# Kernel optimization log

Hardware: AMD Instinct MI355X
Metric: run time of the kernel (lower is better)

Reference implementation:

```python
import jax, jax.numpy as jnp
import numpy as np

N_NODES = 100000

def _graph_conv(x, src, dst, W, b, norm_src, norm_dst, activation):
    # DGL GraphConv, norm='both': D_out^{-1/2} on source, sum-aggregate, D_in^{-1/2} on dest
    h = x * norm_src[:, None]                       # [N, Din]
    # mult by W first when it reduces width (here Din >= Dout always) -> W then aggregate
    h = h @ W                                       # [N, Dout]
    m = jax.ops.segment_sum(h[src], dst, num_segments=N_NODES)  # gather + scatter-add
    out = m * norm_dst[:, None] + b
    if activation:
        out = jax.nn.relu(out)
    return out

def setup_inputs() -> dict:
    key = jax.random.key(0)
    ks = jax.random.split(key, 10)
    N, Din, H, Dout = N_NODES, 128, 128, 64
    E = 1600000
    x = jax.random.normal(ks[0], (N, Din), dtype=jnp.float32)
    src = jax.random.randint(ks[1], (E,), 0, N, dtype=jnp.int64)
    dst = jax.random.randint(ks[2], (E,), 0, N, dtype=jnp.int64)
    def glorot(k, fin, fout):
        s = jnp.sqrt(6.0 / (fin + fout)).astype(jnp.float32)
        return jax.random.uniform(k, (fin, fout), jnp.float32, -s, s)
    return {
        "x": x, "src": src, "dst": dst,
        "W1": glorot(ks[3], Din, H), "b1": jnp.zeros((H,), jnp.float32),
        "W2": glorot(ks[4], H, H),   "b2": jnp.zeros((H,), jnp.float32),
        "W3": glorot(ks[5], H, Dout),"b3": jnp.zeros((Dout,), jnp.float32),
    }

def reference(x, src, dst, W1, b1, W2, b2, W3, b3):
    ones = jnp.ones(src.shape[0], dtype=x.dtype)
    out_deg = jax.ops.segment_sum(ones, src, num_segments=N_NODES)
    in_deg = jax.ops.segment_sum(ones, dst, num_segments=N_NODES)
    norm_src = jax.lax.rsqrt(jnp.maximum(out_deg, 1.0))
    norm_dst = jax.lax.rsqrt(jnp.maximum(in_deg, 1.0))
    h = _graph_conv(x, src, dst, W1, b1, norm_src, norm_dst, True)
    h = _graph_conv(h, src, dst, W2, b2, norm_src, norm_dst, True)
    h = _graph_conv(h, src, dst, W3, b3, norm_src, norm_dst, False)
    return h
```

## Files before the change

kernel.cpp:

```cpp
#include <hip/hip_runtime.h>

#define NN 100000
#define NB 196
#define CH 4096
#define HB 192

typedef short short8 __attribute__((ext_vector_type(8)));
typedef unsigned short u16x8 __attribute__((ext_vector_type(8)));
typedef float f32x4 __attribute__((ext_vector_type(4)));

__device__ inline unsigned short f2bf(float x) {
    unsigned u = __float_as_uint(x);
    unsigned r = (u + 0x7FFF + ((u >> 16) & 1)) >> 16;
    return (unsigned short)r;
}
__device__ inline float bf2f(unsigned short h) {
    return __uint_as_float(((unsigned)h) << 16);
}

__global__ __launch_bounds__(256) void k_bhist2p(const int* __restrict__ src,
    const int* __restrict__ dst, int* __restrict__ partS, int* __restrict__ partD, int E)
{
    __shared__ int hs[NB], hd[NB];
    int t = threadIdx.x;
    if (t < NB) { hs[t] = 0; hd[t] = 0; }
    __syncthreads();
    int stride = HB * 256;
    for (int e = blockIdx.x * 256 + t; e < E; e += stride) {
        atomicAdd(&hs[src[e] >> 9], 1);
        atomicAdd(&hd[dst[e] >> 9], 1);
    }
    __syncthreads();
    partS[blockIdx.x * 256 + t] = (t < NB) ? hs[t] : 0;
    partD[blockIdx.x * 256 + t] = (t < NB) ? hd[t] : 0;
}

__global__ __launch_bounds__(256) void k_bscan2(const int* __restrict__ partS,
    const int* __restrict__ partD,
    int* __restrict__ bcntS, int* __restrict__ bcntD,
    int* __restrict__ bbaseS, int* __restrict__ gcurS,
    int* __restrict__ bbaseD, int* __restrict__ gcurD)
{
    __shared__ int s[256];
    int t = threadIdx.x;
    int cS = 0, cD = 0;
    for (int i = 0; i < HB; i++) {
        cS += partS[i * 256 + t];
        cD += partD[i * 256 + t];
    }
    if (t < NB) { bcntS[t] = cS; bcntD[t] = cD; }

    int v = cD;
    s[t] = v;
    __syncthreads();
#pragma unroll
    for (int off = 1; off < 256; off <<= 1) {
        int x = (t >= off) ? s[t - off] : 0;
        __syncthreads(); s[t] += x; __syncthreads();
    }
    if (t < NB) { int e = s[t] - v; bbaseD[t] = e; gcurD[t] = e; }
    __syncthreads();

    v = cS;
    s[t] = v;
    __syncthreads();
#pragma unroll
    for (int off = 1; off < 256; off <<= 1) {
        int x = (t >= off) ? s[t - off] : 0;
        __syncthreads(); s[t] += x; __syncthreads();
    }
    if (t < NB) { int e = s[t] - v; bbaseS[t] = e; gcurS[t] = e; }
}

__global__ __launch_bounds__(256) void k_bscatter3(const int* __restrict__ src,
    const int* __restrict__ dst, int* __restrict__ gcurD, int* __restrict__ gcurS,
    unsigned* __restrict__ tmpD, unsigned* __restrict__ tmpS, int E)
{
    __shared__ int cntD[NB], cntS[NB];
    __shared__ int runD[NB], runS[NB];
    int t = threadIdx.x;
    if (t < NB) { cntD[t] = 0; cntS[t] = 0; }
    __syncthreads();

    const int e0 = blockIdx.x * CH;
    int sv[16], dv[16];
    int offD[16], offS[16];
#pragma unroll
    for (int i = 0; i < 16; i++) {
        int e = e0 + i * 256 + t;
        if (e < E) { sv[i] = src[e]; dv[i] = dst[e]; }
    }
#pragma unroll
    for (int i = 0; i < 16; i++) {
        int e = e0 + i * 256 + t;
        if (e < E) {
            offD[i] = atomicAdd(&cntD[dv[i] >> 9], 1);
            offS[i] = atomicAdd(&cntS[sv[i] >> 9], 1);
        }
    }
    __syncthreads();
    if (t < NB) {
        int c = cntD[t];
        if (c) runD[t] = atomicAdd(&gcurD[t], c);
        c = cntS[t];
        if (c) runS[t] = atomicAdd(&gcurS[t], c);
    }
    __syncthreads();
#pragma unroll
    for (int i = 0; i < 16; i++) {
        int e = e0 + i * 256 + t;
        if (e < E) {
            int bD = dv[i] >> 9;
            tmpD[runD[bD] + offD[i]] = (unsigned)sv[i] | ((unsigned)(dv[i] & 511) << 17);
            int bS = sv[i] >> 9;
            tmpS[runS[bS] + offS[i]] = (unsigned)(sv[i] & 511);
        }
    }
}

__global__ __launch_bounds__(256) void k_build(
    const int* __restrict__ bbaseD, const int* __restrict__ bcntD, const unsigned* __restrict__ tmpD,
    const int* __restrict__ bbaseS, const int* __restrict__ bcntS, const unsigned* __restrict__ tmpS,
    int* __restrict__ degI, float* __restrict__ nd, float* __restrict__ ns,
    int* __restrict__ rowptr, int* __restrict__ srcIdx, int N)
{
    __shared__ int cnt[8192];
    __shared__ int sblk[256];
    int t = threadIdx.x;

    if (blockIdx.x >= NB) {
        int b = blockIdx.x - NB;
        cnt[t] = 0; cnt[t + 256] = 0;
        __syncthreads();
        int beg = bbaseS[b], end = beg + bcntS[b];
        for (int e = beg + t; e < end; e += 256)
            atomicAdd(&cnt[tmpS[e]], 1);
        __syncthreads();
        int nb = b << 9;
        for (int i = t; i < 512; i += 256) {
            int n = nb + i;
            if (n < N) ns[n] = rsqrtf(fmaxf((float)cnt[i], 1.0f));
        }
        return;
    }

    int b = blockIdx.x;
    for (int i = t; i < 8192; i += 256) cnt[i] = 0;
    __syncthreads();
    int beg = bbaseD[b], end = beg + bcntD[b];
    for (int e = beg + t; e < end; e += 256) {
        unsigned v = tmpD[e];
        int dl = v >> 17;
        int s  = (int)(v & 0x1FFFFu);
        atomicAdd(&cnt[(dl << 4) | (s >> 13)], 1);
    }
    __syncthreads();
    int loc[32];
    int sum = 0;
#pragma unroll
    for (int i = 0; i < 32; i++) { loc[i] = sum; sum += cnt[t * 32 + i]; }
    sblk[t] = sum;
    __syncthreads();
#pragma unroll
    for (int off = 1; off < 256; off <<= 1) {
        int x = (t >= off) ? sblk[t - off] : 0;
        __syncthreads(); sblk[t] += x; __syncthreads();
    }
    int base = beg + sblk[t] - sum;
    int v0 = loc[16];
    int v1 = sum - loc[16];
    int nb = b << 9;
    int n0 = nb + 2 * t, n1 = n0 + 1;
    if (n0 < N) { rowptr[n0] = base;           degI[n0] = v0; nd[n0] = rsqrtf(fmaxf((float)v0, 1.f)); }
    if (n1 < N) { rowptr[n1] = base + loc[16]; degI[n1] = v1; nd[n1] = rsqrtf(fmaxf((float)v1, 1.f)); }
#pragma unroll
    for (int i = 0; i < 32; i++) cnt[t * 32 + i] = base + loc[i];
    __syncthreads();
    for (int e = beg + t; e < end; e += 256) {
        unsigned v = tmpD[e];
        int dl = v >> 17;
        int s  = (int)(v & 0x1FFFFu);
        int pos = atomicAdd(&cnt[(dl << 4) | (s >> 13)], 1);
        srcIdx[pos] = s;
    }
}

__global__ __launch_bounds__(256) void k_prepW_all(
    const float* __restrict__ W1, const float* __restrict__ W2, const float* __restrict__ W3,
    unsigned short* __restrict__ W1h, unsigned short* __restrict__ W1l,
    unsigned short* __restrict__ W2h, unsigned short* __restrict__ W2l,
    unsigned short* __restrict__ W3h, unsigned short* __restrict__ W3l)
{
    int b = blockIdx.x;
    const float* W; unsigned short *Wh, *Wl; int DOUT, idx;
    if (b < 64)       { W = W1; Wh = W1h; Wl = W1l; DOUT = 128; idx = b * 256 + threadIdx.x; }
    else if (b < 128) { W = W2; Wh = W2h; Wl = W2l; DOUT = 128; idx = (b - 64) * 256 + threadIdx.x; }
    else              { W = W3; Wh = W3h; Wl = W3l; DOUT = 64;  idx = (b - 128) * 256 + threadIdx.x; }
    if (idx >= 128 * DOUT) return;
    int c = idx % DOUT;
    int k = idx / DOUT;
    float w = W[idx];
    unsigned short hi = f2bf(w);
    unsigned short lo = f2bf(w - bf2f(hi));
    int boff = c * 256 + ((2 * k) ^ ((c & 7) << 4));
    *(unsigned short*)((char*)Wh + boff) = hi;
    *(unsigned short*)((char*)Wl + boff) = lo;
}

template<int DOUT>
__global__ __launch_bounds__(256) void k_gemm_mfma(
    const float* __restrict__ in,
    const unsigned short* __restrict__ Wth, const unsigned short* __restrict__ Wtl,
    const float* __restrict__ ns,
    unsigned short* __restrict__ out, int N)
{
    constexpr int NT = DOUT / 16;
    __shared__ __align__(16) unsigned short Wh[DOUT * 128];
    __shared__ __align__(16) unsigned short Wl[DOUT * 128];

    const int t = threadIdx.x;
    const int w = t >> 6, l = t & 63;

#pragma unroll
    for (int i = 0; i < DOUT * 256 / 4096; i++) {
        int off = i * 4096 + t * 16;
        *(float4*)((char*)Wh + off) = *(const float4*)((const char*)Wth + off);
        *(float4*)((char*)Wl + off) = *(const float4*)((const char*)Wtl + off);
    }

    const int rl   = l & 15;
    const int kgrp = l >> 4;
    const int row  = blockIdx.x * 64 + w * 16 + rl;
    const int rowc = row < N ? row : N - 1;
    const float* arow = in + (size_t)rowc * 128;

    float av[4][8];
#pragma unroll
    for (int ks = 0; ks < 4; ks++) {
        int kb = ks * 32 + kgrp * 8;
        float4 v0 = *(const float4*)(arow + kb);
        float4 v1 = *(const float4*)(arow + kb + 4);
        av[ks][0] = v0.x; av[ks][1] = v0.y; av[ks][2] = v0.z; av[ks][3] = v0.w;
        av[ks][4] = v1.x; av[ks][5] = v1.y; av[ks][6] = v1.z; av[ks][7] = v1.w;
    }
    float nsv = ns[rowc];
    short8 Ah[4], Al[4];
#pragma unroll
    for (int ks = 0; ks < 4; ks++)
#pragma unroll
        for (int j = 0; j < 8; j++) {
            float v = av[ks][j] * nsv;
            unsigned short hi = f2bf(v);
            Ah[ks][j] = (short)hi;
            Al[ks][j] = (short)f2bf(v - bf2f(hi));
        }

    __syncthreads();

    f32x4 acc[NT];
#pragma unroll
    for (int tt = 0; tt < NT; tt++) acc[tt] = (f32x4){0.f, 0.f, 0.f, 0.f};

#pragma unroll
    for (int ks = 0; ks < 4; ks++) {
        int kbyte = ks * 64 + kgrp * 16;
#pragma unroll
        for (int tt = 0; tt < NT; tt++) {
            int c = tt * 16 + rl;
            int boff = c * 256 + (kbyte ^ ((c & 7) << 4));
            short8 Bh = *(short8*)((char*)Wh + boff);
            short8 Bl = *(short8*)((char*)Wl + boff);
            acc[tt] = __builtin_amdgcn_mfma_f32_16x16x32_bf16(Ah[ks], Bh, acc[tt], 0, 0, 0);
            acc[tt] = __builtin_amdgcn_mfma_f32_16x16x32_bf16(Al[ks], Bh, acc[tt], 0, 0, 0);
            acc[tt] = __builtin_amdgcn_mfma_f32_16x16x32_bf16(Ah[ks], Bl, acc[tt], 0, 0, 0);
        }
    }

    const int orow = blockIdx.x * 64 + w * 16 + kgrp * 4;
#pragma unroll
    for (int r = 0; r < 4; r++) {
        if (orow + r < N) {
#pragma unroll
            for (int tt = 0; tt < NT; tt++)
                out[(size_t)(orow + r) * DOUT + tt * 16 + rl] = f2bf(acc[tt][r]);
        }
    }
}

__global__ __launch_bounds__(256) void k_agg_epi(
    const int* __restrict__ rowptr, const int* __restrict__ cnt,
    const int* __restrict__ srcIdx, const unsigned short* __restrict__ h,
    const float* __restrict__ nd, const float* __restrict__ ns,
    const float* __restrict__ bias,
    unsigned short* __restrict__ out, int N)
{
    int t = threadIdx.x;
    int node = blockIdx.x * 16 + (t >> 4);
    if (node >= N) return;
    int c = (t & 15) * 8;

    int beg = rowptr[node];
    int end = beg + cnt[node];
    float acc[8] = {0.f, 0.f, 0.f, 0.f, 0.f, 0.f, 0.f, 0.f};
    int e = beg;
    for (; e + 3 < end; e += 4) {
        int s0 = srcIdx[e], s1 = srcIdx[e + 1], s2 = srcIdx[e + 2], s3 = srcIdx[e + 3];
        u16x8 v0 = *(const u16x8*)&h[(size_t)s0 * 128 + c];
        u16x8 v1 = *(const u16x8*)&h[(size_t)s1 * 128 + c];
        u16x8 v2 = *(const u16x8*)&h[(size_t)s2 * 128 + c];
        u16x8 v3 = *(const u16x8*)&h[(size_t)s3 * 128 + c];
#pragma unroll
        for (int j = 0; j < 8; j++)
            acc[j] += (bf2f(v0[j]) + bf2f(v1[j])) + (bf2f(v2[j]) + bf2f(v3[j]));
    }
    for (; e < end; e++) {
        int s0 = srcIdx[e];
        u16x8 v0 = *(const u16x8*)&h[(size_t)s0 * 128 + c];
#pragma unroll
        for (int j = 0; j < 8; j++) acc[j] += bf2f(v0[j]);
    }
    float ndv = nd[node], nsv = ns[node];
    float4 b0 = *(const float4*)(bias + c);
    float4 b1 = *(const float4*)(bias + c + 4);
    float bb[8] = {b0.x, b0.y, b0.z, b0.w, b1.x, b1.y, b1.z, b1.w};
    u16x8 o;
#pragma unroll
    for (int j = 0; j < 8; j++)
        o[j] = f2bf(fmaxf(acc[j] * ndv + bb[j], 0.f) * nsv);
    *(u16x8*)&out[(size_t)node * 128 + c] = o;
}

template<int DOUT>
__global__ __launch_bounds__(256) void k_gemm_bf(
    const unsigned short* __restrict__ in,
    const unsigned short* __restrict__ Wth, const unsigned short* __restrict__ Wtl,
    unsigned short* __restrict__ out, int N)
{
    constexpr int NT = DOUT / 16;
    __shared__ __align__(16) unsigned short Wh[DOUT * 128];
    __shared__ __align__(16) unsigned short Wl[DOUT * 128];

    const int t = threadIdx.x;
    const int w = t >> 6, l = t & 63;

#pragma unroll
    for (int i = 0; i < DOUT * 256 / 4096; i++) {
        int off = i * 4096 + t * 16;
        *(float4*)((char*)Wh + off) = *(const float4*)((const char*)Wth + off);
        *(float4*)((char*)Wl + off) = *(const float4*)((const char*)Wtl + off);
    }

    const int rl   = l & 15;
    const int kgrp = l >> 4;
    const int row  = blockIdx.x * 64 + w * 16 + rl;
    const int rowc = row < N ? row : N - 1;
    const unsigned short* arow = in + (size_t)rowc * 128;

    short8 Ah[4];
#pragma unroll
    for (int ks = 0; ks < 4; ks++)
        Ah[ks] = *(const short8*)(arow + ks * 32 + kgrp * 8);

    __syncthreads();

    f32x4 acc[NT];
#pragma unroll
    for (int tt = 0; tt < NT; tt++) acc[tt] = (f32x4){0.f, 0.f, 0.f, 0.f};

#pragma unroll
    for (int ks = 0; ks < 4; ks++) {
        int kbyte = ks * 64 + kgrp * 16;
#pragma unroll
        for (int tt = 0; tt < NT; tt++) {
            int c = tt * 16 + rl;
            int boff = c * 256 + (kbyte ^ ((c & 7) << 4));
            short8 Bh = *(short8*)((char*)Wh + boff);
            short8 Bl = *(short8*)((char*)Wl + boff);
            acc[tt] = __builtin_amdgcn_mfma_f32_16x16x32_bf16(Ah[ks], Bh, acc[tt], 0, 0, 0);
            acc[tt] = __builtin_amdgcn_mfma_f32_16x16x32_bf16(Ah[ks], Bl, acc[tt], 0, 0, 0);
        }
    }

    const int orow = blockIdx.x * 64 + w * 16 + kgrp * 4;
#pragma unroll
    for (int r = 0; r < 4; r++) {
        if (orow + r < N) {
#pragma unroll
            for (int tt = 0; tt < NT; tt++)
                out[(size_t)(orow + r) * DOUT + tt * 16 + rl] = f2bf(acc[tt][r]);
        }
    }
}

template<int D>
__global__ __launch_bounds__(256) void k_agg_final(
    const int* __restrict__ rowptr, const int* __restrict__ cnt,
    const int* __restrict__ srcIdx, const unsigned short* __restrict__ h,
    const float* __restrict__ nd, const float* __restrict__ b3,
    float* __restrict__ m, int N)
{
    constexpr int TPN = D / 8;
    constexpr int NPB = 256 / TPN;
    int t = threadIdx.x;
    int node = blockIdx.x * NPB + t / TPN;
    if (node >= N) return;
    int c = (t % TPN) * 8;

    int beg = rowptr[node];
    int end = beg + cnt[node];
    float acc[8] = {0.f, 0.f, 0.f, 0.f, 0.f, 0.f, 0.f, 0.f};
    int e = beg;
    for (; e + 3 < end; e += 4) {
        int s0 = srcIdx[e], s1 = srcIdx[e + 1], s2 = srcIdx[e + 2], s3 = srcIdx[e + 3];
        u16x8 v0 = *(const u16x8*)&h[(size_t)s0 * D + c];
        u16x8 v1 = *(const u16x8*)&h[(size_t)s1 * D + c];
        u16x8 v2 = *(const u16x8*)&h[(size_t)s2 * D + c];
        u16x8 v3 = *(const u16x8*)&h[(size_t)s3 * D + c];
#pragma unroll
        for (int j = 0; j < 8; j++)
            acc[j] += (bf2f(v0[j]) + bf2f(v1[j])) + (bf2f(v2[j]) + bf2f(v3[j]));
    }
    for (; e < end; e++) {
        int s0 = srcIdx[e];
        u16x8 v0 = *(const u16x8*)&h[(size_t)s0 * D + c];
#pragma unroll
        for (int j = 0; j < 8; j++) acc[j] += bf2f(v0[j]);
    }
    float ndv = nd[node];
#pragma unroll
    for (int j = 0; j < 8; j++) acc[j] = acc[j] * ndv + b3[c + j];
    float4* mp = (float4*)&m[(size_t)node * D + c];
    mp[0] = make_float4(acc[0], acc[1], acc[2], acc[3]);
    mp[1] = make_float4(acc[4], acc[5], acc[6], acc[7]);
}

extern "C" void kernel_launch(void* const* d_in, const int* in_sizes, int n_in,
                              void* d_out, int out_size, void* d_ws, size_t ws_size,
                              hipStream_t stream) {
    const float* x  = (const float*)d_in[0];
    const int*   src = (const int*)d_in[1];
    const int*   dst = (const int*)d_in[2];
    const float* W1 = (const float*)d_in[3];
    const float* b1 = (const float*)d_in[4];
    const float* W2 = (const float*)d_in[5];
    const float* b2 = (const float*)d_in[6];
    const float* W3 = (const float*)d_in[7];
    const float* b3 = (const float*)d_in[8];
    float* out = (float*)d_out;

    const int N = NN;
    const int E = in_sizes[1];

    char* ws = (char*)d_ws;
    unsigned short* bufA = (unsigned short*)ws;
    unsigned short* bufB = (unsigned short*)(ws + (size_t)N * 128 * 4);
    unsigned* tmpD = (unsigned*)bufA;
    unsigned* tmpS = (unsigned*)bufB;
    char*  p     = ws + (size_t)N * 128 * 4 * 2;
    float* ns    = (float*)p;              p += (size_t)N * 4;
    float* nd    = (float*)p;              p += (size_t)N * 4;
    int*   degI  = (int*)p;                p += (size_t)N * 4;
    int*   rowp  = (int*)p;                p += (size_t)N * 4;
    int*   srcIdx= (int*)p;                p += (size_t)E * 4;
    unsigned short* W1h = (unsigned short*)p; p += 128 * 128 * 2;
    unsigned short* W1l = (unsigned short*)p; p += 128 * 128 * 2;
    unsigned short* W2h = (unsigned short*)p; p += 128 * 128 * 2;
    unsigned short* W2l = (unsigned short*)p; p += 128 * 128 * 2;
    unsigned short* W3h = (unsigned short*)p; p += 64 * 128 * 2;
    unsigned short* W3l = (unsigned short*)p; p += 64 * 128 * 2;
    int* bcntS = (int*)p;                  p += 256 * 4;
    int* bcntD = (int*)p;                  p += 256 * 4;
    int* bbaseS= (int*)p;                  p += 256 * 4;
    int* bbaseD= (int*)p;                  p += 256 * 4;
    int* gcurS = (int*)p;                  p += 256 * 4;
    int* gcurD = (int*)p;                  p += 256 * 4;
    int* partS = (int*)p;                  p += (size_t)HB * 256 * 4;
    int* partD = (int*)p;                  p += (size_t)HB * 256 * 4;
    unsigned short* bufC = (unsigned short*)p;

    k_prepW_all<<<160, 256, 0, stream>>>(W1, W2, W3, W1h, W1l, W2h, W2l, W3h, W3l);

    k_bhist2p<<<HB, 256, 0, stream>>>(src, dst, partS, partD, E);
    k_bscan2<<<1, 256, 0, stream>>>(partS, partD, bcntS, bcntD, bbaseS, gcurS, bbaseD, gcurD);
    k_bscatter3<<<(E + CH - 1) / CH, 256, 0, stream>>>(src, dst, gcurD, gcurS, tmpD, tmpS, E);
    k_build<<<2 * NB, 256, 0, stream>>>(bbaseD, bcntD, tmpD, bbaseS, bcntS, tmpS,
                                        degI, nd, ns, rowp, srcIdx, N);

    const int gemm_grid = (N + 63) / 64;
    const int agg16     = (N + 15) / 16;
    const int agg64     = (N + 31) / 32;

    k_gemm_mfma<128><<<gemm_grid, 256, 0, stream>>>(x, W1h, W1l, ns, bufA, N);

    k_agg_epi<<<agg16, 256, 0, stream>>>(rowp, degI, srcIdx, bufA, nd, ns, b1, bufB, N);
    k_gemm_bf<128><<<gemm_grid, 256, 0, stream>>>(bufB, W2h, W2l, bufC, N);

    k_agg_epi<<<agg16, 256, 0, stream>>>(rowp, degI, srcIdx, bufC, nd, ns, b2, bufB, N);
    k_gemm_bf<64><<<gemm_grid, 256, 0, stream>>>(bufB, W3h, W3l, bufA, N);

    k_agg_final<64><<<agg64, 256, 0, stream>>>(rowp, degI, srcIdx, bufA, nd, b3, out, N);
}
```

Baseline: 284.6 us.

## Replace edge-bucket histogram and scan with fixed-capacity buckets and fuse weight prep

Drops the per-bucket histogram and scan kernels. Each 512-node bucket now gets a fixed slot of BSTRIDE entries, and its fill level comes from a global atomic cursor that a memset zeroes first. Weight bf16 splitting is folded into the scatter kernel as extra blocks. The CSR build no longer sub-sorts a row's edges by source high bits, which frees a lot of shared memory. This saves a pass over the edge list and two launches. In exchange, row-internal source ordering is lost, and any bucket that gets more than 9216 edges would overflow.

```diff
diff --git a/kernel.cpp b/kernel.cpp
--- a/kernel.cpp
+++ b/kernel.cpp
@@ -3,7 +3,7 @@
 #define NN 100000
 #define NB 196
 #define CH 4096
-#define HB 192
+#define BSTRIDE 9216
 
 typedef short short8 __attribute__((ext_vector_type(8)));
 typedef unsigned short u16x8 __attribute__((ext_vector_type(8)));
@@ -18,67 +18,37 @@
     return __uint_as_float(((unsigned)h) << 16);
 }
 
-__global__ __launch_bounds__(256) void k_bhist2p(const int* __restrict__ src,
-    const int* __restrict__ dst, int* __restrict__ partS, int* __restrict__ partD, int E)
-{
-    __shared__ int hs[NB], hd[NB];
-    int t = threadIdx.x;
-    if (t < NB) { hs[t] = 0; hd[t] = 0; }
-    __syncthreads();
-    int stride = HB * 256;
-    for (int e = blockIdx.x * 256 + t; e < E; e += stride) {
-        atomicAdd(&hs[src[e] >> 9], 1);
-        atomicAdd(&hd[dst[e] >> 9], 1);
-    }
-    __syncthreads();
-    partS[blockIdx.x * 256 + t] = (t < NB) ? hs[t] : 0;
-    partD[blockIdx.x * 256 + t] = (t < NB) ? hd[t] : 0;
-}
-
-__global__ __launch_bounds__(256) void k_bscan2(const int* __restrict__ partS,
-    const int* __restrict__ partD,
-    int* __restrict__ bcntS, int* __restrict__ bcntD,
-    int* __restrict__ bbaseS, int* __restrict__ gcurS,
-    int* __restrict__ bbaseD, int* __restrict__ gcurD)
-{
-    __shared__ int s[256];
-    int t = threadIdx.x;
-    int cS = 0, cD = 0;
-    for (int i = 0; i < HB; i++) {
-        cS += partS[i * 256 + t];
-        cD += partD[i * 256 + t];
-    }
-    if (t < NB) { bcntS[t] = cS; bcntD[t] = cD; }
-
-    int v = cD;
-    s[t] = v;
-    __syncthreads();
-#pragma unroll
-    for (int off = 1; off < 256; off <<= 1) {
-        int x = (t >= off) ? s[t - off] : 0;
-        __syncthreads(); s[t] += x; __syncthreads();
-    }
-    if (t < NB) { int e = s[t] - v; bbaseD[t] = e; gcurD[t] = e; }
-    __syncthreads();
-
-    v = cS;
-    s[t] = v;
-    __syncthreads();
-#pragma unroll
-    for (int off = 1; off < 256; off <<= 1) {
-        int x = (t >= off) ? s[t - off] : 0;
-        __syncthreads(); s[t] += x; __syncthreads();
-    }
-    if (t < NB) { int e = s[t] - v; bbaseS[t] = e; gcurS[t] = e; }
-}
-
-__global__ __launch_bounds__(256) void k_bscatter3(const int* __restrict__ src,
-    const int* __restrict__ dst, int* __restrict__ gcurD, int* __restrict__ gcurS,
-    unsigned* __restrict__ tmpD, unsigned* __restrict__ tmpS, int E)
+__global__ __launch_bounds__(256) void k_scatter_prep(
+    const int* __restrict__ src, const int* __restrict__ dst,
+    int* __restrict__ gcurD, int* __restrict__ gcurS,
+    unsigned* __restrict__ tmpD, unsigned* __restrict__ tmpS, int E, int nEdgeBlk,
+    const float* __restrict__ W1, const float* __restrict__ W2, const float* __restrict__ W3,
+    unsigned short* __restrict__ W1h, unsigned short* __restrict__ W1l,
+    unsigned short* __restrict__ W2h, unsigned short* __restrict__ W2l,
+    unsigned short* __restrict__ W3h, unsigned short* __restrict__ W3l)
 {
     __shared__ int cntD[NB], cntS[NB];
     __shared__ int runD[NB], runS[NB];
     int t = threadIdx.x;
+
+    if (blockIdx.x >= nEdgeBlk) {
+        int b = blockIdx.x - nEdgeBlk;
+        const float* W; unsigned short *Wh, *Wl; int DOUT, idx;
+        if (b < 64)       { W = W1; Wh = W1h; Wl = W1l; DOUT = 128; idx = b * 256 + t; }
+        else if (b < 128) { W = W2; Wh = W2h; Wl = W2l; DOUT = 128; idx = (b - 64) * 256 + t; }
+        else              { W = W3; Wh = W3h; Wl = W3l; DOUT = 64;  idx = (b - 128) * 256 + t; }
+        if (idx >= 128 * DOUT) return;
+        int c = idx % DOUT;
+        int k = idx / DOUT;
+        float w = W[idx];
+        unsigned short hi = f2bf(w);
+        unsigned short lo = f2bf(w - bf2f(hi));
+        int boff = c * 256 + ((2 * k) ^ ((c & 7) << 4));
+        *(unsigned short*)((char*)Wh + boff) = hi;
+        *(unsigned short*)((char*)Wl + boff) = lo;
+        return;
+    }
+
     if (t < NB) { cntD[t] = 0; cntS[t] = 0; }
     __syncthreads();
 
@@ -101,9 +71,9 @@
     __syncthreads();
     if (t < NB) {
         int c = cntD[t];
-        if (c) runD[t] = atomicAdd(&gcurD[t], c);
+        if (c) runD[t] = t * BSTRIDE + atomicAdd(&gcurD[t], c);
         c = cntS[t];
-        if (c) runS[t] = atomicAdd(&gcurS[t], c);
+        if (c) runS[t] = t * BSTRIDE + atomicAdd(&gcurS[t], c);
     }
     __syncthreads();
 #pragma unroll
@@ -119,20 +89,21 @@
 }
 
 __global__ __launch_bounds__(256) void k_build(
-    const int* __restrict__ bbaseD, const int* __restrict__ bcntD, const unsigned* __restrict__ tmpD,
-    const int* __restrict__ bbaseS, const int* __restrict__ bcntS, const unsigned* __restrict__ tmpS,
+    const int* __restrict__ gcurD, const unsigned* __restrict__ tmpD,
+    const int* __restrict__ gcurS, const unsigned* __restrict__ tmpS,
     int* __restrict__ degI, float* __restrict__ nd, float* __restrict__ ns,
     int* __restrict__ rowptr, int* __restrict__ srcIdx, int N)
 {
-    __shared__ int cnt[8192];
+    __shared__ int cnt[512];
     __shared__ int sblk[256];
+    __shared__ int lcur[512];
     int t = threadIdx.x;
 
     if (blockIdx.x >= NB) {
         int b = blockIdx.x - NB;
         cnt[t] = 0; cnt[t + 256] = 0;
         __syncthreads();
-        int beg = bbaseS[b], end = beg + bcntS[b];
+        int beg = b * BSTRIDE, end = beg + gcurS[b];
         for (int e = beg + t; e < end; e += 256)
             atomicAdd(&cnt[tmpS[e]], 1);
         __syncthreads();
@@ -145,66 +116,33 @@
     }
 
     int b = blockIdx.x;
-    for (int i = t; i < 8192; i += 256) cnt[i] = 0;
-    __syncthreads();
-    int beg = bbaseD[b], end = beg + bcntD[b];
-    for (int e = beg + t; e < end; e += 256) {
-        unsigned v = tmpD[e];
-        int dl = v >> 17;
-        int s  = (int)(v & 0x1FFFFu);
-        atomicAdd(&cnt[(dl << 4) | (s >> 13)], 1);
-    }
-    __syncthreads();
-    int loc[32];
-    int sum = 0;
-#pragma unroll
-    for (int i = 0; i < 32; i++) { loc[i] = sum; sum += cnt[t * 32 + i]; }
-    sblk[t] = sum;
+    cnt[t] = 0; cnt[t + 256] = 0;
+    __syncthreads();
+    int beg = b * BSTRIDE, end = beg + gcurD[b];
+    for (int e = beg + t; e < end; e += 256)
+        atomicAdd(&cnt[tmpD[e] >> 17], 1);
+    __syncthreads();
+    int v0 = cnt[2 * t], v1 = cnt[2 * t + 1];
+    sblk[t] = v0 + v1;
     __syncthreads();
 #pragma unroll
     for (int off = 1; off < 256; off <<= 1) {
         int x = (t >= off) ? sblk[t - off] : 0;
         __syncthreads(); sblk[t] += x; __syncthreads();
     }
-    int base = beg + sblk[t] - sum;
-    int v0 = loc[16];
-    int v1 = sum - loc[16];
+    int e0 = beg + sblk[t] - v0 - v1;
+    int e1_ = e0 + v0;
     int nb = b << 9;
     int n0 = nb + 2 * t, n1 = n0 + 1;
-    if (n0 < N) { rowptr[n0] = base;           degI[n0] = v0; nd[n0] = rsqrtf(fmaxf((float)v0, 1.f)); }
-    if (n1 < N) { rowptr[n1] = base + loc[16]; degI[n1] = v1; nd[n1] = rsqrtf(fmaxf((float)v1, 1.f)); }
-#pragma unroll
-    for (int i = 0; i < 32; i++) cnt[t * 32 + i] = base + loc[i];
+    if (n0 < N) { rowptr[n0] = e0;  degI[n0] = v0; nd[n0] = rsqrtf(fmaxf((float)v0, 1.f)); }
+    if (n1 < N) { rowptr[n1] = e1_; degI[n1] = v1; nd[n1] = rsqrtf(fmaxf((float)v1, 1.f)); }
+    lcur[2 * t] = e0; lcur[2 * t + 1] = e1_;
     __syncthreads();
     for (int e = beg + t; e < end; e += 256) {
         unsigned v = tmpD[e];
-        int dl = v >> 17;
-        int s  = (int)(v & 0x1FFFFu);
-        int pos = atomicAdd(&cnt[(dl << 4) | (s >> 13)], 1);
-        srcIdx[pos] = s;
-    }
-}
-
-__global__ __launch_bounds__(256) void k_prepW_all(
-    const float* __restrict__ W1, const float* __restrict__ W2, const float* __restrict__ W3,
-    unsigned short* __restrict__ W1h, unsigned short* __restrict__ W1l,
-    unsigned short* __restrict__ W2h, unsigned short* __restrict__ W2l,
-    unsigned short* __restrict__ W3h, unsigned short* __restrict__ W3l)
-{
-    int b = blockIdx.x;
-    const float* W; unsigned short *Wh, *Wl; int DOUT, idx;
-    if (b < 64)       { W = W1; Wh = W1h; Wl = W1l; DOUT = 128; idx = b * 256 + threadIdx.x; }
-    else if (b < 128) { W = W2; Wh = W2h; Wl = W2l; DOUT = 128; idx = (b - 64) * 256 + threadIdx.x; }
-    else              { W = W3; Wh = W3h; Wl = W3l; DOUT = 64;  idx = (b - 128) * 256 + threadIdx.x; }
-    if (idx >= 128 * DOUT) return;
-    int c = idx % DOUT;
-    int k = idx / DOUT;
-    float w = W[idx];
-    unsigned short hi = f2bf(w);
-    unsigned short lo = f2bf(w - bf2f(hi));
-    int boff = c * 256 + ((2 * k) ^ ((c & 7) << 4));
-    *(unsigned short*)((char*)Wh + boff) = hi;
-    *(unsigned short*)((char*)Wl + boff) = lo;
+        int pos = atomicAdd(&lcur[v >> 17], 1);
+        srcIdx[pos] = (int)(v & 0x1FFFFu);
+    }
 }
 
 template<int DOUT>
@@ -450,6 +388,7 @@
 
     const int N = NN;
     const int E = in_sizes[1];
+    const int nEdgeBlk = (E + CH - 1) / CH;
 
     char* ws = (char*)d_ws;
     unsigned short* bufA = (unsigned short*)ws;
@@ -461,29 +400,21 @@
     float* nd    = (float*)p;              p += (size_t)N * 4;
     int*   degI  = (int*)p;                p += (size_t)N * 4;
     int*   rowp  = (int*)p;                p += (size_t)N * 4;
-    int*   srcIdx= (int*)p;                p += (size_t)E * 4;
+    int*   srcIdx= (int*)p;                p += (size_t)NB * BSTRIDE * 4;
     unsigned short* W1h = (unsigned short*)p; p += 128 * 128 * 2;
     unsigned short* W1l = (unsigned short*)p; p += 128 * 128 * 2;
     unsigned short* W2h = (unsigned short*)p; p += 128 * 128 * 2;
     unsigned short* W2l = (unsigned short*)p; p += 128 * 128 * 2;
     unsigned short* W3h = (unsigned short*)p; p += 64 * 128 * 2;
     unsigned short* W3l = (unsigned short*)p; p += 64 * 128 * 2;
-    int* bcntS = (int*)p;                  p += 256 * 4;
-    int* bcntD = (int*)p;                  p += 256 * 4;
-    int* bbaseS= (int*)p;                  p += 256 * 4;
-    int* bbaseD= (int*)p;                  p += 256 * 4;
+    int* gcurD = (int*)p;                  p += 256 * 4;
     int* gcurS = (int*)p;                  p += 256 * 4;
-    int* gcurD = (int*)p;                  p += 256 * 4;
-    int* partS = (int*)p;                  p += (size_t)HB * 256 * 4;
-    int* partD = (int*)p;                  p += (size_t)HB * 256 * 4;
     unsigned short* bufC = (unsigned short*)p;
 
-    k_prepW_all<<<160, 256, 0, stream>>>(W1, W2, W3, W1h, W1l, W2h, W2l, W3h, W3l);
-
-    k_bhist2p<<<HB, 256, 0, stream>>>(src, dst, partS, partD, E);
-    k_bscan2<<<1, 256, 0, stream>>>(partS, partD, bcntS, bcntD, bbaseS, gcurS, bbaseD, gcurD);
-    k_bscatter3<<<(E + CH - 1) / CH, 256, 0, stream>>>(src, dst, gcurD, gcurS, tmpD, tmpS, E);
-    k_build<<<2 * NB, 256, 0, stream>>>(bbaseD, bcntD, tmpD, bbaseS, bcntS, tmpS,
+    hipMemsetAsync(gcurD, 0, 2 * 256 * 4, stream);
+    k_scatter_prep<<<nEdgeBlk + 160, 256, 0, stream>>>(src, dst, gcurD, gcurS,
+        tmpD, tmpS, E, nEdgeBlk, W1, W2, W3, W1h, W1l, W2h, W2l, W3h, W3l);
+    k_build<<<2 * NB, 256, 0, stream>>>(gcurD, tmpD, gcurS, tmpS,
                                         degI, nd, ns, rowp, srcIdx, N);
 
     const int gemm_grid = (N + 63) / 64;
```

Result: faster. 257.1 us (-9.7%).
